# Optimization experiments

Hardware: AMD Instinct MI355X
Metric: run time of the kernel (lower is better)

Reference implementation:

```python
import jax, jax.numpy as jnp
import numpy as np

N_BASES = 128
SEG = 3200
N_FFT = 512
HOP = 160
LAM = 0.5          # lambda_sparse
TAU = 10.0
ITERS = 50
N_FREQ = N_FFT // 2 + 1                      # 257
N_FRAMES = (SEG - N_FFT) // HOP + 1          # 17
SPEC_DIM = N_FREQ * N_FRAMES                 # 4369
BATCH = 8192


def setup_inputs() -> dict:
    key = jax.random.key(0)
    k1, k2 = jax.random.split(key)
    audio = jax.random.normal(k1, (BATCH, SEG), dtype=jnp.float32)
    D = jax.random.normal(k2, (N_BASES, SPEC_DIM), dtype=jnp.float32)
    D = D / jnp.linalg.norm(D, axis=1, keepdims=True)  # unit-norm rows, as in _init_dictionary
    return {"audio": audio, "dictionary": D}


def _softshrink(u, lam):
    return jnp.sign(u) * jnp.maximum(jnp.abs(u) - lam, 0.0)


def reference(audio, dictionary):
    B = audio.shape[0]
    # STFT (center=False, periodic hann window), magnitude — matches torch.stft
    window = 0.5 * (1.0 - jnp.cos(2.0 * jnp.pi * jnp.arange(N_FFT, dtype=jnp.float32) / N_FFT))
    idx = jnp.arange(N_FRAMES)[:, None] * HOP + jnp.arange(N_FFT)[None, :]  # (T, n_fft)
    frames = audio[:, idx] * window                      # (B, T, n_fft)
    spec = jnp.abs(jnp.fft.rfft(frames, axis=-1))        # (B, T, F)
    spec = jnp.transpose(spec, (0, 2, 1))                # (B, F, T) — torch.stft layout
    spec_flat = spec.reshape(B, -1)                      # (B, spec_dim)

    # per-sample normalization (stats_initialized=False path); torch std is unbiased
    spec_flat = spec_flat - spec_flat.mean(axis=-1, keepdims=True)
    spec_flat = spec_flat / (jnp.std(spec_flat, axis=-1, ddof=1, keepdims=True) + 1e-8)

    # LCA inference
    gram = dictionary @ dictionary.T - jnp.eye(N_BASES, dtype=dictionary.dtype)
    b = spec_flat @ dictionary.T                         # (B, n_bases)

    def step(u, _):
        a = _softshrink(u, LAM)
        u = u + (b - u - a @ gram) / TAU
        return u, None

    u0 = jnp.zeros((B, N_BASES), dtype=spec_flat.dtype)
    u, _ = jax.lax.scan(step, u0, None, length=ITERS)
    return _softshrink(u, LAM)
```

## Files before the change

### kernel.cpp

```cpp
#include <hip/hip_runtime.h>
#include <hip/hip_bf16.h>
#include <math.h>


typedef short bf16x8 __attribute__((ext_vector_type(8)));
typedef float f32x4  __attribute__((ext_vector_type(4)));

#define TWO_PI_OVER_512 0.01227184630f
#define TWO_PI_OVER_64  0.09817477042f

__device__ __forceinline__ unsigned short f2bf(float f){
  unsigned int u = __float_as_uint(f);
  u += 0x7FFFu + ((u >> 16) & 1u);
  return (unsigned short)(u >> 16);
}
__device__ __forceinline__ float sshrink(float u){
  float a = fabsf(u) - 0.5f;
  return a > 0.0f ? copysignf(a, u) : 0.0f;
}
__device__ __forceinline__ int slot(int i){ return i + (i >> 3) + 5*(i >> 6); }

__global__ __launch_bounds__(256) void k_dprep(const float* __restrict__ D,
    unsigned short* __restrict__ Dbf, float* __restrict__ rowsum){
  __shared__ float row[4369];
  __shared__ float rs[256];
  const int n = blockIdx.x, tid = threadIdx.x;
  float acc = 0.0f;
  for (int k = tid; k < 4369; k += 256){
    float v = D[(size_t)n*4369 + k];
    row[k] = v;
    acc += v;
  }
  rs[tid] = acc;
  __syncthreads();
  #pragma unroll
  for (int s = 128; s > 0; s >>= 1){
    if (tid < s) rs[tid] += rs[tid + s];
    __syncthreads();
  }
  if (tid == 0) rowsum[n] = rs[0];
  for (int i = tid; i < 1096; i += 256){
    int k0 = i*4;
    ushort4 pk;
    unsigned short v[4];
    #pragma unroll
    for (int u = 0; u < 4; u++){
      int kp = k0 + u;
      unsigned short r = 0;
      if (kp < 4369){
        int t = kp / 257, f = kp - t*257;
        r = f2bf(row[f*17 + t]);
      }
      v[u] = r;
    }
    pk.x = v[0]; pk.y = v[1]; pk.z = v[2]; pk.w = v[3];
    *(ushort4*)(Dbf + (size_t)n*4384 + k0) = pk;
  }
}

__global__ __launch_bounds__(64) void k_gram_mm(const unsigned short* __restrict__ Dbf,
    float* __restrict__ pgram){
  const int x = blockIdx.x;
  const int ks = blockIdx.y;
  const int lane = threadIdx.x;
  const int c = lane & 15, q = lane >> 4;
  const unsigned short* ap = Dbf + (size_t)(x*16 + c)*4384 + q*8;
  const unsigned short* bp = Dbf + (size_t)c*4384 + q*8;
  const int t0 = ks*17, t1 = (ks == 7) ? 137 : t0 + 17;
  f32x4 acc[8];
  #pragma unroll
  for (int nt = 0; nt < 8; nt++) acc[nt] = (f32x4){0.f,0.f,0.f,0.f};
  for (int tt = t0; tt < t1; tt++){
    const int k0 = tt*32;
    bf16x8 af = *(const bf16x8*)(ap + k0);
    #pragma unroll
    for (int nt = 0; nt < 8; nt++){
      bf16x8 bfr = *(const bf16x8*)(bp + (size_t)nt*16*4384 + k0);
      acc[nt] = __builtin_amdgcn_mfma_f32_16x16x32_bf16(af, bfr, acc[nt], 0, 0, 0);
    }
  }
  #pragma unroll
  for (int nt = 0; nt < 8; nt++)
    #pragma unroll
    for (int r = 0; r < 4; r++)
      pgram[(size_t)(ks*128 + x*16 + q*4 + r)*128 + nt*16 + c] = acc[nt][r];
}
__global__ __launch_bounds__(128) void k_gram_fin(const float* __restrict__ pgram,
    unsigned short* __restrict__ gram_bf){
  const int x = blockIdx.x, y = threadIdx.x;
  float g = ((pgram[(size_t)x*128+y]        + pgram[(size_t)(128+x)*128+y])
          +  (pgram[(size_t)(256+x)*128+y]  + pgram[(size_t)(384+x)*128+y]))
          + ((pgram[(size_t)(512+x)*128+y]  + pgram[(size_t)(640+x)*128+y])
          +  (pgram[(size_t)(768+x)*128+y]  + pgram[(size_t)(896+x)*128+y]));
  if (x == y) g -= 1.0f;
  gram_bf[x*136 + y] = f2bf(g);
}

__device__ __forceinline__ void dft8(float xr[8], float xi[8]){
  const float C = 0.70710678118654752f;
  float t0r = xr[0]+xr[4], t0i = xi[0]+xi[4];
  float t1r = xr[0]-xr[4], t1i = xi[0]-xi[4];
  float t2r = xr[2]+xr[6], t2i = xi[2]+xi[6];
  float t3r = xr[2]-xr[6], t3i = xi[2]-xi[6];
  float e0r = t0r+t2r, e0i = t0i+t2i;
  float e2r = t0r-t2r, e2i = t0i-t2i;
  float e1r = t1r+t3i, e1i = t1i-t3r;
  float e3r = t1r-t3i, e3i = t1i+t3r;
  float s0r = xr[1]+xr[5], s0i = xi[1]+xi[5];
  float s1r = xr[1]-xr[5], s1i = xi[1]-xi[5];
  float s2r = xr[3]+xr[7], s2i = xi[3]+xi[7];
  float s3r = xr[3]-xr[7], s3i = xi[3]-xi[7];
  float o0r = s0r+s2r, o0i = s0i+s2i;
  float o2r = s0r-s2r, o2i = s0i-s2i;
  float o1r = s1r+s3i, o1i = s1i-s3r;
  float o3r = s1r-s3i, o3i = s1i+s3r;
  xr[0] = e0r+o0r; xi[0] = e0i+o0i;
  xr[4] = e0r-o0r; xi[4] = e0i-o0i;
  float w1r = C*(o1r+o1i), w1i = C*(o1i-o1r);
  xr[1] = e1r+w1r; xi[1] = e1i+w1i;
  xr[5] = e1r-w1r; xi[5] = e1i-w1i;
  xr[2] = e2r+o2i; xi[2] = e2i-o2r;
  xr[6] = e2r-o2i; xi[6] = e2i+o2r;
  float w3r = C*(o3i-o3r), w3i = -C*(o3r+o3i);
  xr[3] = e3r+w3r; xi[3] = e3i+w3i;
  xr[7] = e3r-w3r; xi[7] = e3i-w3i;
}

__global__ __launch_bounds__(256) void k_stft(const float* __restrict__ audio,
    unsigned short* __restrict__ spec, float* __restrict__ sums){
  __shared__ float2 zb[4][616];
  const int wid = threadIdx.x >> 6;
  const int L = threadIdx.x & 63;
  float2* Z = zb[wid];
  const int pair = blockIdx.x*4 + wid;
  const int fr0 = pair*2;
  const int b0 = fr0/17, t0 = fr0 - b0*17;
  const int fr1 = fr0 + 1;
  const int b1 = fr1/17, t1 = fr1 - b1*17;
  const float* sA = audio + (size_t)b0*3200 + t0*160;
  const float* sB = audio + (size_t)b1*3200 + t1*160;
  float xr[8], xi[8];
  {
    const int baseRev = ((L & 7) << 3) | (L >> 3);
    #pragma unroll
    for (int e = 0; e < 8; e++){
      int r9 = baseRev + (e << 6);
      float w = 0.5f - 0.5f*__cosf((float)r9 * TWO_PI_OVER_512);
      xr[e] = sA[r9]*w;
      xi[e] = sB[r9]*w;
    }
  }
  dft8(xr, xi);
  {
    int s0 = 9*L + 5*(L >> 3);
    #pragma unroll
    for (int e = 0; e < 8; e++) Z[s0 + e] = make_float2(xr[e], xi[e]);
  }
  {
    int j = L & 7, g = L >> 3;
    int sb = 77*g + j;
    #pragma unroll
    for (int e = 0; e < 8; e++){
      float2 z = Z[sb + 9*e];
      xr[e] = z.x; xi[e] = z.y;
    }
    #pragma unroll
    for (int e = 1; e < 8; e++){
      float t = (float)(j*e) * TWO_PI_OVER_64;
      float cw = __cosf(t), sw = __sinf(t);
      float a = xr[e], b = xi[e];
      xr[e] = a*cw + b*sw;
      xi[e] = b*cw - a*sw;
    }
    dft8(xr, xi);
    #pragma unroll
    for (int e = 0; e < 8; e++) Z[sb + 9*e] = make_float2(xr[e], xi[e]);
  }
  {
    int sb = L + (L >> 3);
    #pragma unroll
    for (int e = 0; e < 8; e++){
      float2 z = Z[sb + 77*e];
      xr[e] = z.x; xi[e] = z.y;
    }
    #pragma unroll
    for (int e = 1; e < 8; e++){
      float t = (float)(L*e) * TWO_PI_OVER_512;
      float cw = __cosf(t), sw = __sinf(t);
      float a = xr[e], b = xi[e];
      xr[e] = a*cw + b*sw;
      xi[e] = b*cw - a*sw;
    }
    dft8(xr, xi);
  }
  float pr[4], pi[4];
  {
    const int partner = (64 - L) & 63;
    #pragma unroll
    for (int f = 0; f < 4; f++){
      pr[f] = __shfl(xr[7-f], partner);
      pi[f] = __shfl(xi[7-f], partner);
    }
    if (L == 0){
      pr[0] = xr[0]; pi[0] = xi[0];
      pr[1] = xr[7]; pi[1] = xi[7];
      pr[2] = xr[6]; pi[2] = xi[6];
      pr[3] = xr[5]; pi[3] = xi[5];
    }
  }
  unsigned short* dA = spec + (size_t)b0*4384 + t0*257;
  unsigned short* dB = spec + (size_t)b1*4384 + t1*257;
  float s1A = 0.f, s2A = 0.f, s1B = 0.f, s2B = 0.f;
  #pragma unroll
  for (int f = 0; f < 4; f++){
    int k = L + 64*f;
    float ar = xr[f] + pr[f], ai = xi[f] - pi[f];
    float br = xi[f] + pi[f], bi = pr[f] - xr[f];
    float magA = 0.5f*sqrtf(ar*ar + ai*ai);
    float magB = 0.5f*sqrtf(br*br + bi*bi);
    dA[k] = f2bf(magA);
    dB[k] = f2bf(magB);
    s1A += magA; s2A += magA*magA;
    s1B += magB; s2B += magB*magB;
  }
  if (L == 0){
    float magA = fabsf(xr[4]);
    float magB = fabsf(xi[4]);
    dA[256] = f2bf(magA);
    dB[256] = f2bf(magB);
    s1A += magA; s2A += magA*magA;
    s1B += magB; s2B += magB*magB;
  }
  #pragma unroll
  for (int off = 32; off > 0; off >>= 1){
    s1A += __shfl_down(s1A, off);
    s2A += __shfl_down(s2A, off);
    s1B += __shfl_down(s1B, off);
    s2B += __shfl_down(s2B, off);
  }
  if (L == 0){
    atomicAdd(&sums[b0], s1A);
    atomicAdd(&sums[8192 + b0], s2A);
    atomicAdd(&sums[b1], s1B);
    atomicAdd(&sums[8192 + b1], s2B);
  }
  if (t0 == 0 && L < 15) spec[(size_t)b0*4384 + 4369 + L] = 0;
  if (t1 == 0 && L < 15) spec[(size_t)b1*4384 + 4369 + L] = 0;
}

__global__ __launch_bounds__(128) void k_gemm(const unsigned short* __restrict__ spec,
    const unsigned short* __restrict__ Dbf, float* __restrict__ part){
  const int mtile = blockIdx.x;
  const int ks = blockIdx.y;
  const int wv = threadIdx.x >> 6;
  const int lane = threadIdx.x & 63;
  const int c = lane & 15, q = lane >> 4;
  const int m0 = mtile*32 + wv*16;
  const unsigned short* ap = spec + (size_t)(m0 + c)*4384 + q*8;
  const unsigned short* bp = Dbf + (size_t)c*4384 + q*8;
  const int t0 = ks*35, t1 = (ks == 3) ? 137 : (ks*35 + 35);
  f32x4 acc[8];
  #pragma unroll
  for (int nt = 0; nt < 8; nt++) acc[nt] = (f32x4){0.f,0.f,0.f,0.f};
  int k0 = t0*32;
  bf16x8 aC = *(const bf16x8*)(ap + k0);
  bf16x8 bC[8];
  #pragma unroll
  for (int nt = 0; nt < 8; nt++)
    bC[nt] = *(const bf16x8*)(bp + (size_t)nt*16*4384 + k0);
  for (int tt = t0; tt < t1; tt++){
    const int tn = (tt + 1 < t1) ? tt + 1 : tt;
    const int kn = tn*32;
    bf16x8 aN = *(const bf16x8*)(ap + kn);
    bf16x8 bN[8];
    #pragma unroll
    for (int nt = 0; nt < 8; nt++)
      bN[nt] = *(const bf16x8*)(bp + (size_t)nt*16*4384 + kn);
    #pragma unroll
    for (int nt = 0; nt < 8; nt++)
      acc[nt] = __builtin_amdgcn_mfma_f32_16x16x32_bf16(aC, bC[nt], acc[nt], 0, 0, 0);
    aC = aN;
    #pragma unroll
    for (int nt = 0; nt < 8; nt++) bC[nt] = bN[nt];
  }
  float* base = part + (size_t)ks*1048576 + m0 + q*4;
  #pragma unroll
  for (int nt = 0; nt < 8; nt++)
    *(f32x4*)(base + (size_t)(nt*16 + c)*8192) = acc[nt];
}

__global__ __launch_bounds__(256) void k_lca(const float* __restrict__ part,
    const unsigned short* __restrict__ gram_bf, const float* __restrict__ rowsum,
    const float* __restrict__ sums, float* __restrict__ out){
  __shared__ unsigned short A[2][16*136];
  const int tid = threadIdx.x, wv = tid >> 6, lane = tid & 63;
  const int c = lane & 15, q = lane >> 4;
  const int sg = blockIdx.x*16 + c;
  const float S1 = sums[sg], S2 = sums[8192 + sg];
  const float mus = S1 / 4369.0f;
  float var = (S2 - S1*S1/4369.0f) / 4368.0f;
  var = fmaxf(var, 0.0f);
  const float invs = 1.0f / (sqrtf(var) + 1e-8f);
  const int nb = wv*32;
  bf16x8 Gf[2][4];
  #pragma unroll
  for (int rt = 0; rt < 2; rt++)
    #pragma unroll
    for (int kt = 0; kt < 4; kt++)
      Gf[rt][kt] = *(const bf16x8*)(gram_bf + (size_t)(nb + rt*16 + c)*136 + kt*32 + q*8);
  f32x4 U[2], Bb[2];
  #pragma unroll
  for (int rt = 0; rt < 2; rt++){
    #pragma unroll
    for (int r = 0; r < 4; r++){
      int n = nb + rt*16 + q*4 + r;
      float S = part[(size_t)n*8192 + sg]
              + part[(size_t)1048576 + (size_t)n*8192 + sg]
              + part[(size_t)2097152 + (size_t)n*8192 + sg]
              + part[(size_t)3145728 + (size_t)n*8192 + sg];
      Bb[rt][r] = invs * (S - mus * rowsum[n]);
      U[rt][r] = 0.0f;
    }
  }
  for (int it = 0; it < 50; it++){
    unsigned short* Ab = A[it & 1];
    #pragma unroll
    for (int rt = 0; rt < 2; rt++){
      ushort4 pk;
      pk.x = f2bf(sshrink(U[rt][0]));
      pk.y = f2bf(sshrink(U[rt][1]));
      pk.z = f2bf(sshrink(U[rt][2]));
      pk.w = f2bf(sshrink(U[rt][3]));
      *(ushort4*)(Ab + c*136 + nb + rt*16 + q*4) = pk;
    }
    __syncthreads();
    bf16x8 af[4];
    #pragma unroll
    for (int kt = 0; kt < 4; kt++)
      af[kt] = *(const bf16x8*)(Ab + c*136 + kt*32 + q*8);
    f32x4 R[2];
    R[0] = (f32x4){0.f,0.f,0.f,0.f};
    R[1] = (f32x4){0.f,0.f,0.f,0.f};
    #pragma unroll
    for (int kt = 0; kt < 4; kt++)
      #pragma unroll
      for (int rt = 0; rt < 2; rt++)
        R[rt] = __builtin_amdgcn_mfma_f32_16x16x32_bf16(Gf[rt][kt], af[kt], R[rt], 0, 0, 0);
    #pragma unroll
    for (int rt = 0; rt < 2; rt++){
      #pragma unroll
      for (int r = 0; r < 4; r++){
        float u = U[rt][r];
        U[rt][r] = u + (Bb[rt][r] - u - R[rt][r]) * 0.1f;
      }
    }
  }
  #pragma unroll
  for (int rt = 0; rt < 2; rt++){
    float4 o;
    o.x = sshrink(U[rt][0]);
    o.y = sshrink(U[rt][1]);
    o.z = sshrink(U[rt][2]);
    o.w = sshrink(U[rt][3]);
    *(float4*)(out + (size_t)sg*128 + nb + rt*16 + q*4) = o;
  }
}

extern "C" void kernel_launch(void* const* d_in, const int* in_sizes, int n_in,
                              void* d_out, int out_size, void* d_ws, size_t ws_size,
                              hipStream_t stream){
  const float* audio = (const float*)d_in[0];
  const float* D     = (const float*)d_in[1];
  float* out = (float*)d_out;
  char* ws = (char*)d_ws;
  unsigned short* spec   = (unsigned short*)(ws);
  float*          part   = (float*)(ws + 71827456);
  unsigned short* Dbf    = (unsigned short*)(ws + 88604672);
  unsigned short* gram   = (unsigned short*)(ws + 89726976);
  float*          pgram  = (float*)(ws + 89761792);
  float*          rowsum = (float*)(ws + 90286080);
  float*          sums   = (float*)(ws + 90286592);

  hipMemsetAsync(sums, 0, 65536, stream);
  k_stft    <<<17408, 256, 0, stream>>>(audio, spec, sums);
  k_dprep   <<<128, 256, 0, stream>>>(D, Dbf, rowsum);
  k_gram_mm <<<dim3(8, 8, 1), 64, 0, stream>>>(Dbf, pgram);
  k_gram_fin<<<128, 128, 0, stream>>>(pgram, gram);
  k_gemm    <<<dim3(256, 4, 1), 128, 0, stream>>>(spec, Dbf, part);
  k_lca     <<<512, 256, 0, stream>>>(part, gram, rowsum, sums, out);
}
```

Baseline: 333.1 us.

## Use precomputed STFT twiddle/window tables and triple-buffer the GEMM loads

```diff
diff --git a/kernel.cpp b/kernel.cpp
--- a/kernel.cpp
+++ b/kernel.cpp
@@ -7,7 +7,6 @@
 typedef float f32x4  __attribute__((ext_vector_type(4)));
 
 #define TWO_PI_OVER_512 0.01227184630f
-#define TWO_PI_OVER_64  0.09817477042f
 
 __device__ __forceinline__ unsigned short f2bf(float f){
   unsigned int u = __float_as_uint(f);
@@ -18,7 +17,16 @@
   float a = fabsf(u) - 0.5f;
   return a > 0.0f ? copysignf(a, u) : 0.0f;
 }
-__device__ __forceinline__ int slot(int i){ return i + (i >> 3) + 5*(i >> 6); }
+
+__global__ void k_tables(float* __restrict__ wing, float2* __restrict__ twg){
+  int p = blockIdx.x*blockDim.x + threadIdx.x;
+  if (p < 512){
+    int r9 = ((p & 7) << 6) | (p & 56) | (p >> 6);
+    wing[p] = 0.5f - 0.5f*cosf((float)r9 * TWO_PI_OVER_512);
+    float t = (float)p * TWO_PI_OVER_512;
+    twg[p] = make_float2(cosf(t), sinf(t));
+  }
+}
 
 __global__ __launch_bounds__(256) void k_dprep(const float* __restrict__ D,
     unsigned short* __restrict__ Dbf, float* __restrict__ rowsum){
@@ -127,10 +135,17 @@
 }
 
 __global__ __launch_bounds__(256) void k_stft(const float* __restrict__ audio,
+    const float* __restrict__ wing, const float2* __restrict__ twg,
     unsigned short* __restrict__ spec, float* __restrict__ sums){
+  __shared__ float2 twl[512];
+  __shared__ float  winl[512];
   __shared__ float2 zb[4][616];
-  const int wid = threadIdx.x >> 6;
-  const int L = threadIdx.x & 63;
+  const int tid = threadIdx.x;
+  ((float4*)twl)[tid] = ((const float4*)twg)[tid];
+  if (tid < 128) ((float4*)winl)[tid] = ((const float4*)wing)[tid];
+  __syncthreads();
+  const int wid = tid >> 6;
+  const int L = tid & 63;
   float2* Z = zb[wid];
   const int pair = blockIdx.x*4 + wid;
   const int fr0 = pair*2;
@@ -142,12 +157,14 @@
   float xr[8], xi[8];
   {
     const int baseRev = ((L & 7) << 3) | (L >> 3);
+    float4 w0 = *(const float4*)(winl + 8*L);
+    float4 w1 = *(const float4*)(winl + 8*L + 4);
+    float wv[8] = {w0.x,w0.y,w0.z,w0.w,w1.x,w1.y,w1.z,w1.w};
     #pragma unroll
     for (int e = 0; e < 8; e++){
       int r9 = baseRev + (e << 6);
-      float w = 0.5f - 0.5f*__cosf((float)r9 * TWO_PI_OVER_512);
-      xr[e] = sA[r9]*w;
-      xi[e] = sB[r9]*w;
+      xr[e] = sA[r9]*wv[e];
+      xi[e] = sB[r9]*wv[e];
     }
   }
   dft8(xr, xi);
@@ -166,11 +183,10 @@
     }
     #pragma unroll
     for (int e = 1; e < 8; e++){
-      float t = (float)(j*e) * TWO_PI_OVER_64;
-      float cw = __cosf(t), sw = __sinf(t);
+      float2 w = twl[8*j*e];
       float a = xr[e], b = xi[e];
-      xr[e] = a*cw + b*sw;
-      xi[e] = b*cw - a*sw;
+      xr[e] = a*w.x + b*w.y;
+      xi[e] = b*w.x - a*w.y;
     }
     dft8(xr, xi);
     #pragma unroll
@@ -185,11 +201,10 @@
     }
     #pragma unroll
     for (int e = 1; e < 8; e++){
-      float t = (float)(L*e) * TWO_PI_OVER_512;
-      float cw = __cosf(t), sw = __sinf(t);
+      float2 w = twl[L*e];
       float a = xr[e], b = xi[e];
-      xr[e] = a*cw + b*sw;
-      xi[e] = b*cw - a*sw;
+      xr[e] = a*w.x + b*w.y;
+      xi[e] = b*w.x - a*w.y;
     }
     dft8(xr, xi);
   }
@@ -247,6 +262,12 @@
   if (t0 == 0 && L < 15) spec[(size_t)b0*4384 + 4369 + L] = 0;
   if (t1 == 0 && L < 15) spec[(size_t)b1*4384 + 4369 + L] = 0;
 }
+
+#define LDA(dst, tt)  dst = *(const bf16x8*)(ap + (tt)*32)
+#define LDB(dst, tt)  _Pragma("unroll") \
+  for (int nt = 0; nt < 8; nt++) dst[nt] = *(const bf16x8*)(bp + (size_t)nt*16*4384 + (tt)*32)
+#define MM(a, b) _Pragma("unroll") \
+  for (int nt = 0; nt < 8; nt++) acc[nt] = __builtin_amdgcn_mfma_f32_16x16x32_bf16(a, b[nt], acc[nt], 0, 0, 0)
 
 __global__ __launch_bounds__(128) void k_gemm(const unsigned short* __restrict__ spec,
     const unsigned short* __restrict__ Dbf, float* __restrict__ part){
@@ -259,30 +280,25 @@
   const unsigned short* ap = spec + (size_t)(m0 + c)*4384 + q*8;
   const unsigned short* bp = Dbf + (size_t)c*4384 + q*8;
   const int t0 = ks*35, t1 = (ks == 3) ? 137 : (ks*35 + 35);
+  const int tl = t1 - 1;
   f32x4 acc[8];
   #pragma unroll
   for (int nt = 0; nt < 8; nt++) acc[nt] = (f32x4){0.f,0.f,0.f,0.f};
-  int k0 = t0*32;
-  bf16x8 aC = *(const bf16x8*)(ap + k0);
-  bf16x8 bC[8];
-  #pragma unroll
-  for (int nt = 0; nt < 8; nt++)
-    bC[nt] = *(const bf16x8*)(bp + (size_t)nt*16*4384 + k0);
-  for (int tt = t0; tt < t1; tt++){
-    const int tn = (tt + 1 < t1) ? tt + 1 : tt;
-    const int kn = tn*32;
-    bf16x8 aN = *(const bf16x8*)(ap + kn);
-    bf16x8 bN[8];
-    #pragma unroll
-    for (int nt = 0; nt < 8; nt++)
-      bN[nt] = *(const bf16x8*)(bp + (size_t)nt*16*4384 + kn);
-    #pragma unroll
-    for (int nt = 0; nt < 8; nt++)
-      acc[nt] = __builtin_amdgcn_mfma_f32_16x16x32_bf16(aC, bC[nt], acc[nt], 0, 0, 0);
-    aC = aN;
-    #pragma unroll
-    for (int nt = 0; nt < 8; nt++) bC[nt] = bN[nt];
-  }
+  bf16x8 a0, a1, a2, b0[8], b1[8], b2[8];
+  LDA(a0, t0);              LDB(b0, t0);
+  LDA(a1, t0+1);            LDB(b1, t0+1);
+  LDA(a2, t0+2);            LDB(b2, t0+2);
+  int tt = t0;
+  for (; tt + 3 <= t1; tt += 3){
+    int p0 = (tt+3 < t1) ? tt+3 : tl;
+    int p1 = (tt+4 < t1) ? tt+4 : tl;
+    int p2 = (tt+5 < t1) ? tt+5 : tl;
+    MM(a0, b0);  LDA(a0, p0);  LDB(b0, p0);
+    MM(a1, b1);  LDA(a1, p1);  LDB(b1, p1);
+    MM(a2, b2);  LDA(a2, p2);  LDB(b2, p2);
+  }
+  MM(a0, b0);
+  MM(a1, b1);
   float* base = part + (size_t)ks*1048576 + m0 + q*4;
   #pragma unroll
   for (int nt = 0; nt < 8; nt++)
@@ -380,9 +396,12 @@
   float*          pgram  = (float*)(ws + 89761792);
   float*          rowsum = (float*)(ws + 90286080);
   float*          sums   = (float*)(ws + 90286592);
+  float*          wing   = (float*)(ws + 90352128);
+  float2*         twg    = (float2*)(ws + 90354176);
 
   hipMemsetAsync(sums, 0, 65536, stream);
-  k_stft    <<<17408, 256, 0, stream>>>(audio, spec, sums);
+  k_tables  <<<2, 256, 0, stream>>>(wing, twg);
+  k_stft    <<<17408, 256, 0, stream>>>(audio, wing, twg, spec, sums);
   k_dprep   <<<128, 256, 0, stream>>>(D, Dbf, rowsum);
   k_gram_mm <<<dim3(8, 8, 1), 64, 0, stream>>>(Dbf, pgram);
   k_gram_fin<<<128, 128, 0, stream>>>(pgram, gram);
```

Result: slower. 348.2 us (+4.5%).

## Move per-sample spectrum statistics into GEMM via MFMA and use twiddle recurrences

Applied to the files above, without the earlier changes.

```diff
diff --git a/kernel.cpp b/kernel.cpp
--- a/kernel.cpp
+++ b/kernel.cpp
@@ -8,6 +8,7 @@
 
 #define TWO_PI_OVER_512 0.01227184630f
 #define TWO_PI_OVER_64  0.09817477042f
+#define C8 0.70710678118654752f
 
 __device__ __forceinline__ unsigned short f2bf(float f){
   unsigned int u = __float_as_uint(f);
@@ -18,7 +19,6 @@
   float a = fabsf(u) - 0.5f;
   return a > 0.0f ? copysignf(a, u) : 0.0f;
 }
-__device__ __forceinline__ int slot(int i){ return i + (i >> 3) + 5*(i >> 6); }
 
 __global__ __launch_bounds__(256) void k_dprep(const float* __restrict__ D,
     unsigned short* __restrict__ Dbf, float* __restrict__ rowsum){
@@ -127,10 +127,11 @@
 }
 
 __global__ __launch_bounds__(256) void k_stft(const float* __restrict__ audio,
-    unsigned short* __restrict__ spec, float* __restrict__ sums){
+    unsigned short* __restrict__ spec){
   __shared__ float2 zb[4][616];
-  const int wid = threadIdx.x >> 6;
-  const int L = threadIdx.x & 63;
+  const int tid = threadIdx.x;
+  const int wid = tid >> 6;
+  const int L = tid & 63;
   float2* Z = zb[wid];
   const int pair = blockIdx.x*4 + wid;
   const int fr0 = pair*2;
@@ -142,12 +143,16 @@
   float xr[8], xi[8];
   {
     const int baseRev = ((L & 7) << 3) | (L >> 3);
+    float th0 = (float)baseRev * TWO_PI_OVER_512;
+    float cw = __cosf(th0), sw = __sinf(th0);
     #pragma unroll
     for (int e = 0; e < 8; e++){
       int r9 = baseRev + (e << 6);
-      float w = 0.5f - 0.5f*__cosf((float)r9 * TWO_PI_OVER_512);
+      float w = 0.5f - 0.5f*cw;
       xr[e] = sA[r9]*w;
       xi[e] = sB[r9]*w;
+      float nc = C8*(cw - sw), ns = C8*(sw + cw);
+      cw = nc; sw = ns;
     }
   }
   dft8(xr, xi);
@@ -164,13 +169,16 @@
       float2 z = Z[sb + 9*e];
       xr[e] = z.x; xi[e] = z.y;
     }
+    float ang = (float)j * TWO_PI_OVER_64;
+    float c1 = __cosf(ang), s1 = __sinf(ang);
+    float cw = c1, sw = s1;
     #pragma unroll
     for (int e = 1; e < 8; e++){
-      float t = (float)(j*e) * TWO_PI_OVER_64;
-      float cw = __cosf(t), sw = __sinf(t);
       float a = xr[e], b = xi[e];
       xr[e] = a*cw + b*sw;
       xi[e] = b*cw - a*sw;
+      float nc = cw*c1 - sw*s1, ns = sw*c1 + cw*s1;
+      cw = nc; sw = ns;
     }
     dft8(xr, xi);
     #pragma unroll
@@ -183,13 +191,16 @@
       float2 z = Z[sb + 77*e];
       xr[e] = z.x; xi[e] = z.y;
     }
+    float ang = (float)L * TWO_PI_OVER_512;
+    float c1 = __cosf(ang), s1 = __sinf(ang);
+    float cw = c1, sw = s1;
     #pragma unroll
     for (int e = 1; e < 8; e++){
-      float t = (float)(L*e) * TWO_PI_OVER_512;
-      float cw = __cosf(t), sw = __sinf(t);
       float a = xr[e], b = xi[e];
       xr[e] = a*cw + b*sw;
       xi[e] = b*cw - a*sw;
+      float nc = cw*c1 - sw*s1, ns = sw*c1 + cw*s1;
+      cw = nc; sw = ns;
     }
     dft8(xr, xi);
   }
@@ -210,46 +221,25 @@
   }
   unsigned short* dA = spec + (size_t)b0*4384 + t0*257;
   unsigned short* dB = spec + (size_t)b1*4384 + t1*257;
-  float s1A = 0.f, s2A = 0.f, s1B = 0.f, s2B = 0.f;
   #pragma unroll
   for (int f = 0; f < 4; f++){
     int k = L + 64*f;
     float ar = xr[f] + pr[f], ai = xi[f] - pi[f];
     float br = xi[f] + pi[f], bi = pr[f] - xr[f];
-    float magA = 0.5f*sqrtf(ar*ar + ai*ai);
-    float magB = 0.5f*sqrtf(br*br + bi*bi);
-    dA[k] = f2bf(magA);
-    dB[k] = f2bf(magB);
-    s1A += magA; s2A += magA*magA;
-    s1B += magB; s2B += magB*magB;
+    dA[k] = f2bf(0.5f*sqrtf(ar*ar + ai*ai));
+    dB[k] = f2bf(0.5f*sqrtf(br*br + bi*bi));
   }
   if (L == 0){
-    float magA = fabsf(xr[4]);
-    float magB = fabsf(xi[4]);
-    dA[256] = f2bf(magA);
-    dB[256] = f2bf(magB);
-    s1A += magA; s2A += magA*magA;
-    s1B += magB; s2B += magB*magB;
-  }
-  #pragma unroll
-  for (int off = 32; off > 0; off >>= 1){
-    s1A += __shfl_down(s1A, off);
-    s2A += __shfl_down(s2A, off);
-    s1B += __shfl_down(s1B, off);
-    s2B += __shfl_down(s2B, off);
-  }
-  if (L == 0){
-    atomicAdd(&sums[b0], s1A);
-    atomicAdd(&sums[8192 + b0], s2A);
-    atomicAdd(&sums[b1], s1B);
-    atomicAdd(&sums[8192 + b1], s2B);
+    dA[256] = f2bf(fabsf(xr[4]));
+    dB[256] = f2bf(fabsf(xi[4]));
   }
   if (t0 == 0 && L < 15) spec[(size_t)b0*4384 + 4369 + L] = 0;
   if (t1 == 0 && L < 15) spec[(size_t)b1*4384 + 4369 + L] = 0;
 }
 
 __global__ __launch_bounds__(128) void k_gemm(const unsigned short* __restrict__ spec,
-    const unsigned short* __restrict__ Dbf, float* __restrict__ part){
+    const unsigned short* __restrict__ Dbf, float* __restrict__ part,
+    float* __restrict__ psums){
   const int mtile = blockIdx.x;
   const int ks = blockIdx.y;
   const int wv = threadIdx.x >> 6;
@@ -259,9 +249,14 @@
   const unsigned short* ap = spec + (size_t)(m0 + c)*4384 + q*8;
   const unsigned short* bp = Dbf + (size_t)c*4384 + q*8;
   const int t0 = ks*35, t1 = (ks == 3) ? 137 : (ks*35 + 35);
-  f32x4 acc[8];
+  f32x4 acc[8], accS1, accS2;
   #pragma unroll
   for (int nt = 0; nt < 8; nt++) acc[nt] = (f32x4){0.f,0.f,0.f,0.f};
+  accS1 = (f32x4){0.f,0.f,0.f,0.f};
+  accS2 = (f32x4){0.f,0.f,0.f,0.f};
+  bf16x8 onesv;
+  #pragma unroll
+  for (int i = 0; i < 8; i++) onesv[i] = (short)0x3F80;
   int k0 = t0*32;
   bf16x8 aC = *(const bf16x8*)(ap + k0);
   bf16x8 bC[8];
@@ -279,6 +274,8 @@
     #pragma unroll
     for (int nt = 0; nt < 8; nt++)
       acc[nt] = __builtin_amdgcn_mfma_f32_16x16x32_bf16(aC, bC[nt], acc[nt], 0, 0, 0);
+    accS1 = __builtin_amdgcn_mfma_f32_16x16x32_bf16(aC, onesv, accS1, 0, 0, 0);
+    accS2 = __builtin_amdgcn_mfma_f32_16x16x32_bf16(aC, aC,    accS2, 0, 0, 0);
     aC = aN;
     #pragma unroll
     for (int nt = 0; nt < 8; nt++) bC[nt] = bN[nt];
@@ -287,16 +284,23 @@
   #pragma unroll
   for (int nt = 0; nt < 8; nt++)
     *(f32x4*)(base + (size_t)(nt*16 + c)*8192) = acc[nt];
+  if (c == 0)
+    *(f32x4*)(psums + (size_t)ks*8192 + m0 + q*4) = accS1;
+  if ((c >> 2) == q)
+    psums[(size_t)(4 + ks)*8192 + m0 + c] = accS2[c & 3];
 }
 
 __global__ __launch_bounds__(256) void k_lca(const float* __restrict__ part,
     const unsigned short* __restrict__ gram_bf, const float* __restrict__ rowsum,
-    const float* __restrict__ sums, float* __restrict__ out){
+    const float* __restrict__ psums, float* __restrict__ out){
   __shared__ unsigned short A[2][16*136];
   const int tid = threadIdx.x, wv = tid >> 6, lane = tid & 63;
   const int c = lane & 15, q = lane >> 4;
   const int sg = blockIdx.x*16 + c;
-  const float S1 = sums[sg], S2 = sums[8192 + sg];
+  const float S1 = (psums[sg] + psums[8192 + sg])
+                 + (psums[16384 + sg] + psums[24576 + sg]);
+  const float S2 = (psums[32768 + sg] + psums[40960 + sg])
+                 + (psums[49152 + sg] + psums[57344 + sg]);
   const float mus = S1 / 4369.0f;
   float var = (S2 - S1*S1/4369.0f) / 4368.0f;
   var = fmaxf(var, 0.0f);
@@ -379,13 +383,12 @@
   unsigned short* gram   = (unsigned short*)(ws + 89726976);
   float*          pgram  = (float*)(ws + 89761792);
   float*          rowsum = (float*)(ws + 90286080);
-  float*          sums   = (float*)(ws + 90286592);
-
-  hipMemsetAsync(sums, 0, 65536, stream);
-  k_stft    <<<17408, 256, 0, stream>>>(audio, spec, sums);
+  float*          psums  = (float*)(ws + 90286592);
+
+  k_stft    <<<17408, 256, 0, stream>>>(audio, spec);
   k_dprep   <<<128, 256, 0, stream>>>(D, Dbf, rowsum);
   k_gram_mm <<<dim3(8, 8, 1), 64, 0, stream>>>(Dbf, pgram);
   k_gram_fin<<<128, 128, 0, stream>>>(pgram, gram);
-  k_gemm    <<<dim3(256, 4, 1), 128, 0, stream>>>(spec, Dbf, part);
-  k_lca     <<<512, 256, 0, stream>>>(part, gram, rowsum, sums, out);
-}
+  k_gemm    <<<dim3(256, 4, 1), 128, 0, stream>>>(spec, Dbf, part, psums);
+  k_lca     <<<512, 256, 0, stream>>>(part, gram, rowsum, psums, out);
+}
```

Result: faster. 301.8 us (-9.4%).
